# Kernel tuning notes

Hardware: AMD Instinct MI355X
Metric: run time of the kernel (lower is better)

The kernel has to match this reference:

```python
import jax, jax.numpy as jnp
import numpy as np

D_MODEL = 2048
D_FF = 8192
N_LOCAL = 8192


def _ffn(x, W1, b1, W2, b2):
    # ExpertFFN: Linear -> GELU(exact, torch default) -> Linear
    h = jax.nn.gelu(x @ W1 + b1, approximate=False)
    return h @ W2 + b2


def setup_inputs() -> dict:
    key = jax.random.key(0)
    ks = jax.random.split(key, 12)
    s1 = 1.0 / np.sqrt(D_MODEL)
    s2 = 1.0 / np.sqrt(D_FF)
    inp = {
        "x_local": jax.random.normal(ks[0], (N_LOCAL, D_MODEL), jnp.float32),
        "top2_exp_id": jax.random.randint(ks[1], (N_LOCAL, 2), 0, 2),
        "top2_weight": jax.random.uniform(ks[2], (N_LOCAL, 2), jnp.float32),
        # expert 0 params
        "W1_0": jax.random.uniform(ks[3], (D_MODEL, D_FF), jnp.float32, -s1, s1),
        "b1_0": jax.random.uniform(ks[4], (D_FF,), jnp.float32, -s1, s1),
        "W2_0": jax.random.uniform(ks[5], (D_FF, D_MODEL), jnp.float32, -s2, s2),
        "b2_0": jax.random.uniform(ks[6], (D_MODEL,), jnp.float32, -s2, s2),
        # expert 1 params
        "W1_1": jax.random.uniform(ks[7], (D_MODEL, D_FF), jnp.float32, -s1, s1),
        "b1_1": jax.random.uniform(ks[8], (D_FF,), jnp.float32, -s1, s1),
        "W2_1": jax.random.uniform(ks[9], (D_FF, D_MODEL), jnp.float32, -s2, s2),
        "b2_1": jax.random.uniform(ks[10], (D_MODEL,), jnp.float32, -s2, s2),
    }
    return inp


def reference(x_local, top2_exp_id, top2_weight,
              W1_0, b1_0, W2_0, b2_0, W1_1, b1_1, W2_1, b2_1):
    # Single-rank semantics of MoETop2TwoExpertsPerRank (world_size=1):
    # every token is dispatched to its two chosen local experts (ids in {0,1})
    # and results are combined weighted by the gate weights.
    y0 = _ffn(x_local, W1_0, b1_0, W2_0, b2_0)  # (N, d_model)
    y1 = _ffn(x_local, W1_1, b1_1, W2_1, b2_1)  # (N, d_model)
    # local expert id = global_eid % 2 (EPR=2); select per (token, slot)
    sel = (top2_exp_id % 2)[..., None].astype(x_local.dtype)  # (N, 2, 1)
    ys = jnp.stack([y0, y1], axis=1)  # not needed; use where instead
    per_slot = (1.0 - sel) * y0[:, None, :] + sel * y1[:, None, :]  # (N,2,d)
    y_out = jnp.sum(top2_weight[..., None] * per_slot, axis=1)
    return y_out
```

## Files before the change

### kernel.cpp

```cpp
#include <hip/hip_runtime.h>
#include <hip/hip_bf16.h>
#include <stdint.h>

#define DM 2048
#define DF 8192
#define NT 8192

typedef unsigned short u16;
typedef __attribute__((ext_vector_type(8))) __bf16 bf16x8;
typedef __attribute__((ext_vector_type(4))) float f32x4;

typedef __attribute__((address_space(1))) uint8_t ga_u8_t;
typedef __attribute__((address_space(3))) uint8_t lds_u8_t;

__device__ __forceinline__ void async_cp16(const void* g, void* l) {
  __builtin_amdgcn_global_load_lds((ga_u8_t*)g, (lds_u8_t*)l, 16, 0, 0);
}

__device__ __forceinline__ u16 f2b(float f) {
  unsigned int u = __builtin_bit_cast(unsigned int, f);
  u = (u + 0x7fffu + ((u >> 16) & 1u)) >> 16;
  return (u16)u;
}

__device__ __forceinline__ float erf_fast(float z) {
  float az = fabsf(z);
  float t = __builtin_amdgcn_rcpf(fmaf(0.3275911f, az, 1.0f));
  float p = t * fmaf(t, fmaf(t, fmaf(t, fmaf(t, 1.061405429f, -1.453152027f),
                                     1.421413741f), -0.284496736f),
                     0.254829592f);
  float r = fmaf(-p, __expf(-az * az), 1.0f);
  return copysignf(r, z);
}
__device__ __forceinline__ float gelu_f(float x) {
  return 0.5f * x * (1.0f + erf_fast(x * 0.70710678118654752f));
}

__global__ void prep_wtok(const int* __restrict__ eid, const float* __restrict__ w,
                          float2* __restrict__ wtok, int n) {
  int i = blockIdx.x * blockDim.x + threadIdx.x;
  if (i >= n) return;
  float a = 0.f, b = 0.f;
  int e0 = eid[2 * i] & 1, e1 = eid[2 * i + 1] & 1;
  float w0 = w[2 * i], w1 = w[2 * i + 1];
  if (e0) b += w0; else a += w0;
  if (e1) b += w1; else a += w1;
  wtok[i] = make_float2(a, b);
}

__global__ void conv_f32_bf16(const float* __restrict__ in, u16* __restrict__ out,
                              int n4) {
  int i = blockIdx.x * blockDim.x + threadIdx.x;
  if (i >= n4) return;
  float4 v = reinterpret_cast<const float4*>(in)[i];
  ushort4 o;
  o.x = f2b(v.x); o.y = f2b(v.y); o.z = f2b(v.z); o.w = f2b(v.w);
  reinterpret_cast<ushort4*>(out)[i] = o;
}

__global__ void transpose_conv(const float* __restrict__ in, u16* __restrict__ out,
                               int R, int Cc) {
  __shared__ float tile[32][33];
  int tx = threadIdx.x & 31, ty = threadIdx.x >> 5;
  int r0 = blockIdx.y * 32, c0 = blockIdx.x * 32;
#pragma unroll
  for (int i = 0; i < 32; i += 8)
    tile[ty + i][tx] = in[(size_t)(r0 + ty + i) * Cc + c0 + tx];
  __syncthreads();
#pragma unroll
  for (int i = 0; i < 32; i += 8)
    out[(size_t)(c0 + ty + i) * R + r0 + tx] = f2b(tile[tx][ty + i]);
}

__global__ void fill_sentinel(float* p, int n) {
  int i = blockIdx.x * blockDim.x + threadIdx.x;
  if (i < n) p[i] = 0.125f;
}

template <int MODE>
__global__ __launch_bounds__(512, 2)
void gemm_bt(const u16* __restrict__ A, const u16* __restrict__ Bt,
             void* __restrict__ Cv, const float2* __restrict__ wtok,
             const float* __restrict__ bias,
             int M, int N, int K, int sel) {
  __shared__ __align__(16) char smem[131072];
  const int tid = threadIdx.x;
  const int w = tid >> 6;
  const int lane = tid & 63;

  const int nwg = gridDim.x * gridDim.y;
  const int wg = blockIdx.y * gridDim.x + blockIdx.x;
  const int swz = (wg & 7) * (nwg >> 3) + (wg >> 3);
  const int bx = swz % gridDim.x;
  const int by = swz / gridDim.x;
  const int m0 = by * 256;
  const int n0 = bx * 256;
  const int NKT = K >> 6;

  const int r8 = lane >> 3, p8 = lane & 7, q = p8 ^ r8;
  const u16* gA[2];
  const u16* gB[2];
  int ldsOff[2];
#pragma unroll
  for (int j = 0; j < 2; ++j) {
    const int c = j * 8 + w;
    const int row = c * 8 + r8;
    gA[j] = A + (size_t)(m0 + row) * K + q * 8;
    gB[j] = Bt + (size_t)(n0 + row) * K + q * 8;
    ldsOff[j] = c * 1024;
  }
  const size_t hstep = (size_t)128 * K;

  auto stA = [&](int kt, int h, int bp) {
    char* d = smem + bp * 65536 + h * 16384;
    const size_t go = (size_t)h * hstep + (size_t)kt * 64;
    async_cp16(gA[0] + go, d + ldsOff[0]);
    async_cp16(gA[1] + go, d + ldsOff[1]);
  };
  auto stB = [&](int kt, int h, int bp) {
    char* d = smem + 32768 + bp * 65536 + h * 16384;
    const size_t go = (size_t)h * hstep + (size_t)kt * 64;
    async_cp16(gB[0] + go, d + ldsOff[0]);
    async_cp16(gB[1] + go, d + ldsOff[1]);
  };

  const int fr = lane & 15, qw = lane >> 4;
  const int wr = w >> 2, wc = w & 3;
  const int sw = (qw ^ (fr & 7)) << 4;
  const uint32_t aBase = (uint32_t)((wr * 128 + fr) * 128 + sw);
  const uint32_t bBase = (uint32_t)(32768 + (wc * 64 + fr) * 128 + sw);

  auto ldf = [&](const char* base, uint32_t off) {
    return *reinterpret_cast<const bf16x8*>(base + off);
  };

  f32x4 acc[8][4] = {};
  bf16x8 af[4][2], bq[4][2];

  stA(0, 0, 0); stA(0, 1, 0);
  stB(0, 0, 0); stB(0, 1, 0);
  stB(1, 0, 1); stB(1, 1, 1);
  asm volatile("s_waitcnt vmcnt(4)" ::: "memory");
  __builtin_amdgcn_s_barrier();

  for (int t = 0; t < NKT; ++t) {
    const int bp = t & 1;
    const char* Ab = smem + bp * 65536;
    const int kt1 = (t + 1 < NKT) ? t + 1 : NKT - 1;
    const int kt2 = (t + 2 < NKT) ? t + 2 : NKT - 1;

#pragma unroll
    for (int i = 0; i < 4; ++i) {
      af[i][0] = ldf(Ab, aBase + i * 2048);
      af[i][1] = ldf(Ab, (aBase + i * 2048) ^ 64u);
    }
#pragma unroll
    for (int j = 0; j < 2; ++j) {
      bq[j][0] = ldf(Ab, bBase + j * 2048);
      bq[j][1] = ldf(Ab, (bBase + j * 2048) ^ 64u);
    }
    stA(kt1, 0, bp ^ 1);
    asm volatile("s_waitcnt lgkmcnt(0)" ::: "memory");
    __builtin_amdgcn_sched_barrier(0);
    __builtin_amdgcn_s_setprio(1);
#pragma unroll
    for (int kk = 0; kk < 2; ++kk)
#pragma unroll
      for (int i = 0; i < 4; ++i)
#pragma unroll
        for (int j = 0; j < 2; ++j)
          acc[i][j] = __builtin_amdgcn_mfma_f32_16x16x32_bf16(
              bq[j][kk], af[i][kk], acc[i][j], 0, 0, 0);
    __builtin_amdgcn_s_setprio(0);

#pragma unroll
    for (int j = 2; j < 4; ++j) {
      bq[j][0] = ldf(Ab, bBase + j * 2048);
      bq[j][1] = ldf(Ab, (bBase + j * 2048) ^ 64u);
    }
    stA(kt1, 1, bp ^ 1);
    asm volatile("s_waitcnt lgkmcnt(0)" ::: "memory");
    __builtin_amdgcn_sched_barrier(0);
    __builtin_amdgcn_s_setprio(1);
#pragma unroll
    for (int kk = 0; kk < 2; ++kk)
#pragma unroll
      for (int i = 0; i < 4; ++i)
#pragma unroll
        for (int j = 2; j < 4; ++j)
          acc[i][j] = __builtin_amdgcn_mfma_f32_16x16x32_bf16(
              bq[j][kk], af[i][kk], acc[i][j], 0, 0, 0);
    __builtin_amdgcn_s_setprio(0);
    __builtin_amdgcn_s_barrier();
    __builtin_amdgcn_sched_barrier(0);

#pragma unroll
    for (int i = 0; i < 4; ++i) {
      af[i][0] = ldf(Ab, aBase + (i + 4) * 2048);
      af[i][1] = ldf(Ab, (aBase + (i + 4) * 2048) ^ 64u);
    }
    stB(kt2, 0, bp);
    asm volatile("s_waitcnt lgkmcnt(0)" ::: "memory");
    __builtin_amdgcn_sched_barrier(0);
    __builtin_amdgcn_s_setprio(1);
#pragma unroll
    for (int kk = 0; kk < 2; ++kk)
#pragma unroll
      for (int i = 0; i < 4; ++i)
#pragma unroll
        for (int j = 2; j < 4; ++j)
          acc[i + 4][j] = __builtin_amdgcn_mfma_f32_16x16x32_bf16(
              bq[j][kk], af[i][kk], acc[i + 4][j], 0, 0, 0);
    __builtin_amdgcn_s_setprio(0);

    stB(kt2, 1, bp);
    __builtin_amdgcn_s_setprio(1);
#pragma unroll
    for (int kk = 0; kk < 2; ++kk)
#pragma unroll
      for (int i = 0; i < 4; ++i)
#pragma unroll
        for (int j = 0; j < 2; ++j)
          acc[i + 4][j] = __builtin_amdgcn_mfma_f32_16x16x32_bf16(
              bq[j][kk], af[i][kk], acc[i + 4][j], 0, 0, 0);
    __builtin_amdgcn_s_setprio(0);
    asm volatile("s_waitcnt vmcnt(4)" ::: "memory");
    __builtin_amdgcn_s_barrier();
    __builtin_amdgcn_sched_barrier(0);
  }
  asm volatile("s_waitcnt vmcnt(0)" ::: "memory");

#pragma unroll
  for (int i = 0; i < 8; ++i) {
    const int trow = m0 + wr * 128 + i * 16 + fr;
    const float2 wt = wtok[trow];
    const float ws = sel ? wt.y : wt.x;
#pragma unroll
    for (int j = 0; j < 4; ++j) {
      const int col0 = n0 + wc * 64 + j * 16 + qw * 4;
      const float4 bb = *reinterpret_cast<const float4*>(bias + col0);
      f32x4 a = acc[i][j];
      if (MODE == 0) {
        u16* C = (u16*)Cv;
        ushort4 o;
        o.x = f2b(gelu_f(a.x + bb.x) * ws);
        o.y = f2b(gelu_f(a.y + bb.y) * ws);
        o.z = f2b(gelu_f(a.z + bb.z) * ws);
        o.w = f2b(gelu_f(a.w + bb.w) * ws);
        *reinterpret_cast<ushort4*>(C + (size_t)trow * N + col0) = o;
      } else {
        float* C = (float*)Cv;
        float4 o;
        o.x = a.x + ws * bb.x;
        o.y = a.y + ws * bb.y;
        o.z = a.z + ws * bb.z;
        o.w = a.w + ws * bb.w;
        if (MODE == 2) {
          float4 pv = *reinterpret_cast<const float4*>(C + (size_t)trow * N + col0);
          o.x += pv.x; o.y += pv.y; o.z += pv.z; o.w += pv.w;
        }
        *reinterpret_cast<float4*>(C + (size_t)trow * N + col0) = o;
      }
    }
  }
}

extern "C" void kernel_launch(void* const* d_in, const int* in_sizes, int n_in,
                              void* d_out, int out_size, void* d_ws, size_t ws_size,
                              hipStream_t stream) {
  const float* x    = (const float*)d_in[0];
  const int*   eid  = (const int*)d_in[1];
  const float* topw = (const float*)d_in[2];
  const float* W1_0 = (const float*)d_in[3];
  const float* b1_0 = (const float*)d_in[4];
  const float* W2_0 = (const float*)d_in[5];
  const float* b2_0 = (const float*)d_in[6];
  const float* W1_1 = (const float*)d_in[7];
  const float* b1_1 = (const float*)d_in[8];
  const float* W2_1 = (const float*)d_in[9];
  const float* b2_1 = (const float*)d_in[10];
  float* out = (float*)d_out;

  char* ws = (char*)d_ws;
  const size_t SZ_WT = (size_t)DM * DF * sizeof(u16);
  size_t off = (size_t)NT * sizeof(float2);
  float2* wtok = (float2*)ws;
  u16* Xb  = (u16*)(ws + off); off += (size_t)NT * DM * sizeof(u16);
  u16* WTa = (u16*)(ws + off); off += SZ_WT;
  u16* WTb = (u16*)(ws + off); off += SZ_WT;
  u16* H   = (u16*)(ws + off); off += (size_t)NT * DF * sizeof(u16);

  if (ws_size < off) {
    fill_sentinel<<<(out_size + 255) / 256, 256, 0, stream>>>(out, out_size);
    return;
  }

  prep_wtok<<<(NT + 255) / 256, 256, 0, stream>>>(eid, topw, wtok, NT);
  conv_f32_bf16<<<(NT * DM / 4 + 255) / 256, 256, 0, stream>>>(x, Xb, NT * DM / 4);

  dim3 g1(DF / 256, NT / 256);
  dim3 g2(DM / 256, NT / 256);

  transpose_conv<<<dim3(DF / 32, DM / 32), 256, 0, stream>>>(W1_0, WTa, DM, DF);
  gemm_bt<0><<<g1, 512, 0, stream>>>(Xb, WTa, H, wtok, b1_0, NT, DF, DM, 0);
  transpose_conv<<<dim3(DM / 32, DF / 32), 256, 0, stream>>>(W2_0, WTb, DF, DM);
  gemm_bt<1><<<g2, 512, 0, stream>>>(H, WTb, out, wtok, b2_0, NT, DM, DF, 0);
  transpose_conv<<<dim3(DF / 32, DM / 32), 256, 0, stream>>>(W1_1, WTa, DM, DF);
  gemm_bt<0><<<g1, 512, 0, stream>>>(Xb, WTa, H, wtok, b1_1, NT, DF, DM, 1);
  transpose_conv<<<dim3(DM / 32, DF / 32), 256, 0, stream>>>(W2_1, WTb, DF, DM);
  gemm_bt<2><<<g2, 512, 0, stream>>>(H, WTb, out, wtok, b2_1, NT, DM, DF, 1);
}
```

Before: 1.259 ms.

## Reschedule GEMM inner loop by k-half with partial LDS waits; vectorize weight transpose

The GEMM main loop now splits each k-tile into its two k-halves and loads all B fragments for one half at once. MFMA groups then start under partial lgkmcnt waits, so later LDS fragment reads overlap earlier math instead of waiting for every read. The weight transpose/convert kernel moves to 64x64 tiles with float4 loads and ushort4 stores to cut memory transactions. The risks are extra register pressure from the larger fragment sets and hand-counted lgkmcnt values that must match the actual number of outstanding LDS reads.

Result: no change. 1.239 ms (-1.6%).

```diff
diff --git a/kernel.cpp b/kernel.cpp
--- a/kernel.cpp
+++ b/kernel.cpp
@@ -60,16 +60,31 @@
 
 __global__ void transpose_conv(const float* __restrict__ in, u16* __restrict__ out,
                                int R, int Cc) {
-  __shared__ float tile[32][33];
-  int tx = threadIdx.x & 31, ty = threadIdx.x >> 5;
-  int r0 = blockIdx.y * 32, c0 = blockIdx.x * 32;
-#pragma unroll
-  for (int i = 0; i < 32; i += 8)
-    tile[ty + i][tx] = in[(size_t)(r0 + ty + i) * Cc + c0 + tx];
+  __shared__ float tile[64][65];
+  const int tid = threadIdx.x;
+  const int r0 = blockIdx.y * 64, c0 = blockIdx.x * 64;
+  const int ty = tid >> 4;
+  const int tx = (tid & 15) << 2;
+#pragma unroll
+  for (int i = 0; i < 4; ++i) {
+    int r = ty + i * 16;
+    float4 v = *reinterpret_cast<const float4*>(&in[(size_t)(r0 + r) * Cc + c0 + tx]);
+    tile[r][tx] = v.x; tile[r][tx + 1] = v.y;
+    tile[r][tx + 2] = v.z; tile[r][tx + 3] = v.w;
+  }
   __syncthreads();
-#pragma unroll
-  for (int i = 0; i < 32; i += 8)
-    out[(size_t)(c0 + ty + i) * R + r0 + tx] = f2b(tile[tx][ty + i]);
+  const int rg = (tid & 15) << 2;
+  const int cg = tid >> 4;
+#pragma unroll
+  for (int i = 0; i < 4; ++i) {
+    int c = cg + 16 * i;
+    ushort4 o;
+    o.x = f2b(tile[rg + 0][c]);
+    o.y = f2b(tile[rg + 1][c]);
+    o.z = f2b(tile[rg + 2][c]);
+    o.w = f2b(tile[rg + 3][c]);
+    *reinterpret_cast<ushort4*>(&out[(size_t)(c0 + c) * R + r0 + rg]) = o;
+  }
 }
 
 __global__ void fill_sentinel(float* p, int n) {
@@ -135,13 +150,14 @@
   };
 
   f32x4 acc[8][4] = {};
-  bf16x8 af[4][2], bq[4][2];
+  bf16x8 aL[4], aH[4], b0[4], b1[4];
 
   stA(0, 0, 0); stA(0, 1, 0);
   stB(0, 0, 0); stB(0, 1, 0);
   stB(1, 0, 1); stB(1, 1, 1);
   asm volatile("s_waitcnt vmcnt(4)" ::: "memory");
   __builtin_amdgcn_s_barrier();
+  __builtin_amdgcn_sched_barrier(0);
 
   for (int t = 0; t < NKT; ++t) {
     const int bp = t & 1;
@@ -150,80 +166,76 @@
     const int kt2 = (t + 2 < NKT) ? t + 2 : NKT - 1;
 
 #pragma unroll
-    for (int i = 0; i < 4; ++i) {
-      af[i][0] = ldf(Ab, aBase + i * 2048);
-      af[i][1] = ldf(Ab, (aBase + i * 2048) ^ 64u);
-    }
-#pragma unroll
-    for (int j = 0; j < 2; ++j) {
-      bq[j][0] = ldf(Ab, bBase + j * 2048);
-      bq[j][1] = ldf(Ab, (bBase + j * 2048) ^ 64u);
-    }
+    for (int j = 0; j < 4; ++j) b0[j] = ldf(Ab, bBase + j * 2048);
+#pragma unroll
+    for (int i = 0; i < 4; ++i) aL[i] = ldf(Ab, aBase + i * 2048);
+    __builtin_amdgcn_sched_barrier(0);
+#pragma unroll
+    for (int i = 0; i < 4; ++i) aH[i] = ldf(Ab, aBase + (i + 4) * 2048);
+    __builtin_amdgcn_sched_barrier(0);
     stA(kt1, 0, bp ^ 1);
+    asm volatile("s_waitcnt lgkmcnt(4)" ::: "memory");
+    __builtin_amdgcn_sched_barrier(0);
+    __builtin_amdgcn_s_setprio(1);
+#pragma unroll
+    for (int i = 0; i < 4; ++i)
+#pragma unroll
+      for (int j = 0; j < 4; ++j)
+        acc[i][j] = __builtin_amdgcn_mfma_f32_16x16x32_bf16(b0[j], aL[i],
+                                                            acc[i][j], 0, 0, 0);
+    __builtin_amdgcn_s_setprio(0);
+    __builtin_amdgcn_sched_barrier(0);
+
+#pragma unroll
+    for (int j = 0; j < 4; ++j) b1[j] = ldf(Ab, (bBase + j * 2048) ^ 64u);
+#pragma unroll
+    for (int i = 0; i < 4; ++i) aL[i] = ldf(Ab, (aBase + i * 2048) ^ 64u);
+    __builtin_amdgcn_sched_barrier(0);
+    stA(kt1, 1, bp ^ 1);
+    asm volatile("s_waitcnt lgkmcnt(8)" ::: "memory");
+    __builtin_amdgcn_sched_barrier(0);
+    __builtin_amdgcn_s_setprio(1);
+#pragma unroll
+    for (int i = 0; i < 4; ++i)
+#pragma unroll
+      for (int j = 0; j < 4; ++j)
+        acc[i + 4][j] = __builtin_amdgcn_mfma_f32_16x16x32_bf16(b0[j], aH[i],
+                                                                acc[i + 4][j],
+                                                                0, 0, 0);
+    __builtin_amdgcn_s_setprio(0);
+    __builtin_amdgcn_sched_barrier(0);
+
+#pragma unroll
+    for (int i = 0; i < 4; ++i) aH[i] = ldf(Ab, (aBase + (i + 4) * 2048) ^ 64u);
+    __builtin_amdgcn_sched_barrier(0);
+    asm volatile("s_waitcnt lgkmcnt(4)" ::: "memory");
+    __builtin_amdgcn_sched_barrier(0);
+    __builtin_amdgcn_s_barrier();
+    __builtin_amdgcn_sched_barrier(0);
+    stB(kt2, 0, bp);
+    __builtin_amdgcn_s_setprio(1);
+#pragma unroll
+    for (int i = 0; i < 4; ++i)
+#pragma unroll
+      for (int j = 0; j < 4; ++j)
+        acc[i][j] = __builtin_amdgcn_mfma_f32_16x16x32_bf16(b1[j], aL[i],
+                                                            acc[i][j], 0, 0, 0);
+    __builtin_amdgcn_s_setprio(0);
+    __builtin_amdgcn_sched_barrier(0);
+
+    stB(kt2, 1, bp);
     asm volatile("s_waitcnt lgkmcnt(0)" ::: "memory");
     __builtin_amdgcn_sched_barrier(0);
     __builtin_amdgcn_s_setprio(1);
 #pragma unroll
-    for (int kk = 0; kk < 2; ++kk)
-#pragma unroll
-      for (int i = 0; i < 4; ++i)
-#pragma unroll
-        for (int j = 0; j < 2; ++j)
-          acc[i][j] = __builtin_amdgcn_mfma_f32_16x16x32_bf16(
-              bq[j][kk], af[i][kk], acc[i][j], 0, 0, 0);
+    for (int i = 0; i < 4; ++i)
+#pragma unroll
+      for (int j = 0; j < 4; ++j)
+        acc[i + 4][j] = __builtin_amdgcn_mfma_f32_16x16x32_bf16(b1[j], aH[i],
+                                                                acc[i + 4][j],
+                                                                0, 0, 0);
     __builtin_amdgcn_s_setprio(0);
-
-#pragma unroll
-    for (int j = 2; j < 4; ++j) {
-      bq[j][0] = ldf(Ab, bBase + j * 2048);
-      bq[j][1] = ldf(Ab, (bBase + j * 2048) ^ 64u);
-    }
-    stA(kt1, 1, bp ^ 1);
-    asm volatile("s_waitcnt lgkmcnt(0)" ::: "memory");
-    __builtin_amdgcn_sched_barrier(0);
-    __builtin_amdgcn_s_setprio(1);
-#pragma unroll
-    for (int kk = 0; kk < 2; ++kk)
-#pragma unroll
-      for (int i = 0; i < 4; ++i)
-#pragma unroll
-        for (int j = 2; j < 4; ++j)
-          acc[i][j] = __builtin_amdgcn_mfma_f32_16x16x32_bf16(
-              bq[j][kk], af[i][kk], acc[i][j], 0, 0, 0);
-    __builtin_amdgcn_s_setprio(0);
-    __builtin_amdgcn_s_barrier();
-    __builtin_amdgcn_sched_barrier(0);
-
-#pragma unroll
-    for (int i = 0; i < 4; ++i) {
-      af[i][0] = ldf(Ab, aBase + (i + 4) * 2048);
-      af[i][1] = ldf(Ab, (aBase + (i + 4) * 2048) ^ 64u);
-    }
-    stB(kt2, 0, bp);
-    asm volatile("s_waitcnt lgkmcnt(0)" ::: "memory");
-    __builtin_amdgcn_sched_barrier(0);
-    __builtin_amdgcn_s_setprio(1);
-#pragma unroll
-    for (int kk = 0; kk < 2; ++kk)
-#pragma unroll
-      for (int i = 0; i < 4; ++i)
-#pragma unroll
-        for (int j = 2; j < 4; ++j)
-          acc[i + 4][j] = __builtin_amdgcn_mfma_f32_16x16x32_bf16(
-              bq[j][kk], af[i][kk], acc[i + 4][j], 0, 0, 0);
-    __builtin_amdgcn_s_setprio(0);
-
-    stB(kt2, 1, bp);
-    __builtin_amdgcn_s_setprio(1);
-#pragma unroll
-    for (int kk = 0; kk < 2; ++kk)
-#pragma unroll
-      for (int i = 0; i < 4; ++i)
-#pragma unroll
-        for (int j = 0; j < 2; ++j)
-          acc[i + 4][j] = __builtin_amdgcn_mfma_f32_16x16x32_bf16(
-              bq[j][kk], af[i][kk], acc[i + 4][j], 0, 0, 0);
-    __builtin_amdgcn_s_setprio(0);
+    __builtin_amdgcn_sched_barrier(0);
     asm volatile("s_waitcnt vmcnt(4)" ::: "memory");
     __builtin_amdgcn_s_barrier();
     __builtin_amdgcn_sched_barrier(0);
@@ -301,12 +313,12 @@
   dim3 g1(DF / 256, NT / 256);
   dim3 g2(DM / 256, NT / 256);
 
-  transpose_conv<<<dim3(DF / 32, DM / 32), 256, 0, stream>>>(W1_0, WTa, DM, DF);
+  transpose_conv<<<dim3(DF / 64, DM / 64), 256, 0, stream>>>(W1_0, WTa, DM, DF);
   gemm_bt<0><<<g1, 512, 0, stream>>>(Xb, WTa, H, wtok, b1_0, NT, DF, DM, 0);
-  transpose_conv<<<dim3(DM / 32, DF / 32), 256, 0, stream>>>(W2_0, WTb, DF, DM);
+  transpose_conv<<<dim3(DM / 64, DF / 64), 256, 0, stream>>>(W2_0, WTb, DF, DM);
   gemm_bt<1><<<g2, 512, 0, stream>>>(H, WTb, out, wtok, b2_0, NT, DM, DF, 0);
-  transpose_conv<<<dim3(DF / 32, DM / 32), 256, 0, stream>>>(W1_1, WTa, DM, DF);
+  transpose_conv<<<dim3(DF / 64, DM / 64), 256, 0, stream>>>(W1_1, WTa, DM, DF);
   gemm_bt<0><<<g1, 512, 0, stream>>>(Xb, WTa, H, wtok, b1_1, NT, DF, DM, 1);
-  transpose_conv<<<dim3(DM / 32, DF / 32), 256, 0, stream>>>(W2_1, WTb, DF, DM);
+  transpose_conv<<<dim3(DM / 64, DF / 64), 256, 0, stream>>>(W2_1, WTb, DF, DM);
   gemm_bt<2><<<g2, 512, 0, stream>>>(H, WTb, out, wtok, b2_1, NT, DM, DF, 1);
 }
```
